# Kernel optimization log

Measured on AMD Instinct MI355X. Metric: run time of the kernel, lower is better.

Reference implementation:

```python
import jax, jax.numpy as jnp
import numpy as np

N_AE = 512
N_DE = 256
N = 100000
NUM_SEG = 1024
EPS = 1e-5


def setup_inputs() -> dict:
    key = jax.random.key(0)
    ks = jax.random.split(key, 20)
    d_in1 = 2 * N_AE + N_DE  # 1280
    inp = {
        "x": jax.random.normal(ks[0], (N, 2 * N_AE), dtype=jnp.float32),
        "dist_feat": jax.random.normal(ks[1], (N, N_DE), dtype=jnp.float32),
        "atom_idx": jax.random.randint(ks[2], (N,), 0, 100, dtype=jnp.int32),
        "ele_idx": jax.random.randint(ks[3], (N,), 0, NUM_SEG, dtype=jnp.int32),
        # layer 1 params
        "l1_w": jax.random.normal(ks[4], (d_in1, N_AE), dtype=jnp.float32) * (1.0 / np.sqrt(d_in1)),
        "l1_b": jnp.zeros((N_AE,), dtype=jnp.float32),
        "l1_g": jnp.ones((N_AE,), dtype=jnp.float32),
        "l1_be": jnp.zeros((N_AE,), dtype=jnp.float32),
        # layer 2 params (same input width: 2*n_ae + n_de)
        "l2_w": jax.random.normal(ks[5], (d_in1, N_AE), dtype=jnp.float32) * (1.0 / np.sqrt(d_in1)),
        "l2_b": jnp.zeros((N_AE,), dtype=jnp.float32),
        "l2_g": jnp.ones((N_AE,), dtype=jnp.float32),
        "l2_be": jnp.zeros((N_AE,), dtype=jnp.float32),
        # final fc + bn
        "f_w": jax.random.normal(ks[6], (2 * N_AE, N_AE), dtype=jnp.float32) * (1.0 / np.sqrt(2 * N_AE)),
        "f_b": jnp.zeros((N_AE,), dtype=jnp.float32),
        "f_g": jnp.ones((N_AE,), dtype=jnp.float32),
        "f_be": jnp.zeros((N_AE,), dtype=jnp.float32),
    }
    return inp


def _bn(h, gamma, beta):
    # BatchNorm1d in training mode: batch stats, biased variance
    m = jnp.mean(h, axis=0)
    v = jnp.mean(jnp.square(h - m), axis=0)
    return gamma * (h - m) * jax.lax.rsqrt(v + EPS) + beta


def _dist_layer(x_cat, ele_idx, w, b, gamma, beta):
    h = jax.nn.relu(_bn(x_cat @ w + b, gamma, beta))  # [N, n_ae]
    sums = jax.ops.segment_sum(h, ele_idx, num_segments=NUM_SEG)  # [S, n_ae]
    cnt = jax.ops.segment_sum(jnp.ones((h.shape[0],), h.dtype), ele_idx, num_segments=NUM_SEG)
    mean = sums / jnp.maximum(cnt, 1.0)[:, None]
    return jnp.concatenate([h, mean[ele_idx]], axis=1)  # [N, 2*n_ae]


def reference(x, dist_feat, atom_idx, ele_idx,
              l1_w, l1_b, l1_g, l1_be,
              l2_w, l2_b, l2_g, l2_be,
              f_w, f_b, f_g, f_be):
    h = _dist_layer(jnp.concatenate([x, dist_feat], axis=1), ele_idx, l1_w, l1_b, l1_g, l1_be)
    h = _dist_layer(jnp.concatenate([h, dist_feat], axis=1), ele_idx, l2_w, l2_b, l2_g, l2_be)
    out = jax.nn.relu(_bn(h @ f_w + f_b, f_g, f_be))  # [N, n_ae]
    return out
```

## Files before the change

### kernel.cpp

```cpp
#include <hip/hip_runtime.h>
#include <stdint.h>
#include <stdio.h>

#define NOUT 512
#define NSEG 1024

typedef unsigned short u16;
typedef __attribute__((ext_vector_type(4))) float f32x4;
typedef __attribute__((ext_vector_type(8))) short s16x8;
typedef __attribute__((ext_vector_type(4))) unsigned short u16x4;

__device__ __forceinline__ u16 f2b(float f) {
  union { float f; uint32_t u; } v; v.f = f;
  uint32_t r = v.u + 0x7FFFu + ((v.u >> 16) & 1u);
  return (u16)(r >> 16);
}
__device__ __forceinline__ float b2f(u16 b) {
  union { uint32_t u; float f; } v; v.u = ((uint32_t)b) << 16;
  return v.f;
}

typedef __attribute__((address_space(1))) const void GAS;
typedef __attribute__((address_space(3))) void LAS;
__device__ __forceinline__ void llds16(const void* g, void* l) {
  __builtin_amdgcn_global_load_lds((GAS*)g, (LAS*)l, 16, 0, 0);
}

__global__ void k_cast2(const float* __restrict__ x, u16* __restrict__ xb, long n4x,
                        const float* __restrict__ d, u16* __restrict__ db, long n4d) {
  long i0 = blockIdx.x * (long)blockDim.x + threadIdx.x;
  long stride = (long)gridDim.x * blockDim.x;
  for (long i = i0; i < n4x; i += stride) {
    float4 v = reinterpret_cast<const float4*>(x)[i];
    u16x4 o;
    o.x = f2b(v.x); o.y = f2b(v.y); o.z = f2b(v.z); o.w = f2b(v.w);
    reinterpret_cast<u16x4*>(xb)[i] = o;
  }
  for (long i = i0; i < n4d; i += stride) {
    float4 v = reinterpret_cast<const float4*>(d)[i];
    u16x4 o;
    o.x = f2b(v.x); o.y = f2b(v.y); o.z = f2b(v.z); o.w = f2b(v.w);
    reinterpret_cast<u16x4*>(db)[i] = o;
  }
}

__global__ void k_wtcastT3(const float* __restrict__ w0, u16* __restrict__ o0,
                           const float* __restrict__ w1, u16* __restrict__ o1,
                           const float* __restrict__ w2, u16* __restrict__ o2) {
  __shared__ float tile[32][33];
  int z = blockIdx.z;
  const float* w = z == 0 ? w0 : (z == 1 ? w1 : w2);
  u16* out = z == 0 ? o0 : (z == 1 ? o1 : o2);
  int K = z == 2 ? 1024 : 1280;
  int k0 = blockIdx.x * 32, c0 = blockIdx.y * 32;
  if (k0 >= K) return;
  int t = threadIdx.x;
  int rr = t >> 5, cc = t & 31;
#pragma unroll
  for (int p = 0; p < 4; ++p)
    tile[p * 8 + rr][cc] = w[(long)(k0 + p * 8 + rr) * NOUT + c0 + cc];
  __syncthreads();
#pragma unroll
  for (int p = 0; p < 4; ++p)
    out[(long)(c0 + p * 8 + rr) * K + k0 + cc] = f2b(tile[cc][p * 8 + rr]);
}

__global__ void k_hist(const int* __restrict__ ele, int* __restrict__ cnt, int N) {
  int i = blockIdx.x * blockDim.x + threadIdx.x;
  int stride = gridDim.x * blockDim.x;
  for (; i < N; i += stride) atomicAdd(&cnt[ele[i]], 1);
}

__global__ void k_scan(const int* __restrict__ cnt, int* __restrict__ off) {
  __shared__ int tmp[NSEG];
  int t = threadIdx.x;
  tmp[t] = cnt[t];
  __syncthreads();
  for (int o = 1; o < NSEG; o <<= 1) {
    int add = (t >= o) ? tmp[t - o] : 0;
    __syncthreads();
    tmp[t] += add;
    __syncthreads();
  }
  off[t] = tmp[t] - cnt[t];
}

__global__ void k_scatter(const int* __restrict__ ele, const int* __restrict__ off,
                          int* __restrict__ fill, int* __restrict__ rows, int N) {
  int i = blockIdx.x * blockDim.x + threadIdx.x;
  int stride = gridDim.x * blockDim.x;
  for (; i < N; i += stride) {
    int e = ele[i];
    int p = atomicAdd(&fill[e], 1);
    rows[off[e] + p] = i;
  }
}

__global__ void k_bnseg(const u16* __restrict__ hp, u16* __restrict__ h, u16* __restrict__ mean,
                        const float* __restrict__ stats, const float* __restrict__ g,
                        const float* __restrict__ be, float invM,
                        const int* __restrict__ off, const int* __restrict__ cnt,
                        const int* __restrict__ rows) {
  int s = blockIdx.x;
  int c0 = 2 * threadIdx.x;
  int n = cnt[s], o = off[s];
  float m0 = stats[c0] * invM, m1 = stats[c0 + 1] * invM;
  float v0 = stats[NOUT + c0] * invM - m0 * m0;
  float v1 = stats[NOUT + c0 + 1] * invM - m1 * m1;
  float a0 = g[c0] * rsqrtf(v0 + 1e-5f);
  float a1 = g[c0 + 1] * rsqrtf(v1 + 1e-5f);
  float cc0 = be[c0] - a0 * m0;
  float cc1 = be[c0 + 1] - a1 * m1;
  float s0 = 0.f, s1 = 0.f;
#pragma unroll 2
  for (int j = 0; j < n; ++j) {
    int r = rows[o + j];
    uint32_t v = *reinterpret_cast<const uint32_t*>(&hp[(long)r * NOUT + c0]);
    float h0 = fmaxf(a0 * b2f((u16)(v & 0xffff)) + cc0, 0.f);
    float h1 = fmaxf(a1 * b2f((u16)(v >> 16)) + cc1, 0.f);
    s0 += h0; s1 += h1;
    *reinterpret_cast<uint32_t*>(&h[(long)r * NOUT + c0]) =
        ((uint32_t)f2b(h1) << 16) | (uint32_t)f2b(h0);
  }
  float inv = 1.f / fmaxf((float)n, 1.f);
  *reinterpret_cast<uint32_t*>(&mean[(long)s * NOUT + c0]) =
      ((uint32_t)f2b(s1 * inv) << 16) | (uint32_t)f2b(s0 * inv);
}

__global__ void k_final(const u16* __restrict__ hp, float* __restrict__ out,
                        const float* __restrict__ stats, const float* __restrict__ g,
                        const float* __restrict__ be, float invM, long n4) {
  __shared__ float sA[NOUT], sC[NOUT];
  for (int c = threadIdx.x; c < NOUT; c += blockDim.x) {
    float m = stats[c] * invM;
    float v = stats[NOUT + c] * invM - m * m;
    float a = g[c] * rsqrtf(v + 1e-5f);
    sA[c] = a;
    sC[c] = be[c] - a * m;
  }
  __syncthreads();
  long i = blockIdx.x * (long)blockDim.x + threadIdx.x;
  long stride = (long)gridDim.x * blockDim.x;
  for (; i < n4; i += stride) {
    u16x4 v = reinterpret_cast<const u16x4*>(hp)[i];
    int c0 = (int)((i * 4) & (NOUT - 1));
    float4 a = *reinterpret_cast<const float4*>(&sA[c0]);
    float4 c = *reinterpret_cast<const float4*>(&sC[c0]);
    float4 o;
    o.x = fmaxf(a.x * b2f(v.x) + c.x, 0.f);
    o.y = fmaxf(a.y * b2f(v.y) + c.y, 0.f);
    o.z = fmaxf(a.z * b2f(v.z) + c.z, 0.f);
    o.w = fmaxf(a.w * b2f(v.w) + c.w, 0.f);
    reinterpret_cast<float4*>(out)[i] = o;
  }
}

__global__ __launch_bounds__(256, 4) void k_gemm(
    const u16* p0, const u16* p1, int e0, int w0, int w1, int g0, int g1,
    const int* __restrict__ ele,
    const u16* __restrict__ wbt, int ldb, int e0b, int bskip,
    const float* __restrict__ tab, int addtab,
    u16* __restrict__ outp, float* __restrict__ outf, int wf32,
    float* __restrict__ csum, float* __restrict__ csq, int dostats,
    int M, int K) {
  __shared__ __align__(16) u16 As[2 * 4096];
  __shared__ __align__(16) u16 Bs[2 * 4096];

  int nwg = gridDim.x;
  int orig = blockIdx.x;
  int q = nwg >> 3, r8 = nwg & 7;
  int xcd = orig & 7, loc = orig >> 3;
  int bid = (xcd < r8 ? xcd * (q + 1) : r8 * (q + 1) + (xcd - r8) * q) + loc;
  int mt = bid >> 2, ct = bid & 3;
  int brow = mt * 128, bcol = ct * 128;

  int tid = (int)threadIdx.x;
  int lane = tid & 63;
  int wid = tid >> 6;
  int wr = wid >> 1, wc = wid & 1;
  int l15 = lane & 15, kg = lane >> 4;

  int srow = tid >> 2;
  int soct = ((tid & 3) ^ ((srow >> 1) & 3)) * 8;

  int gr0 = brow + srow, gr1 = gr0 + 64;
  int gr0c = gr0 < M ? gr0 : M - 1;
  int gr1c = gr1 < M ? gr1 : M - 1;
  int el0 = ele[gr0c], el1 = ele[gr1c];

  const u16* a00 = p0 + (long)(g0 ? el0 : gr0c) * w0 + soct;
  const u16* a01 = p1 + (long)(g1 ? el0 : gr0c) * w1 + soct - e0;
  const u16* a10 = p0 + (long)(g0 ? el1 : gr1c) * w0 + soct;
  const u16* a11 = p1 + (long)(g1 ? el1 : gr1c) * w1 + soct - e0;

  const u16* b0p = wbt + (long)(bcol + srow) * ldb + soct;
  const u16* b1p = wbt + (long)(bcol + srow + 64) * ldb + soct;

  int xoct = (kg ^ ((l15 >> 1) & 3)) * 8;
  int aro = (wr * 64 + l15) * 32 + xoct;
  int bro = (wc * 64 + l15) * 32 + xoct;

  f32x4 acc[4][4];
#pragma unroll
  for (int m = 0; m < 4; ++m)
#pragma unroll
    for (int n = 0; n < 4; ++n)
#pragma unroll
      for (int j = 0; j < 4; ++j) acc[m][n][j] = 0.f;

  int KT = K >> 5;
  int dst = wid * 512;

  auto stage = [&](int tt, int buf) {
    int k0 = tt << 5;
    const u16* sa0 = k0 < e0 ? a00 : a01;
    const u16* sa1 = k0 < e0 ? a10 : a11;
    int bo = k0 + (k0 >= e0b ? bskip : 0);
    int ab = buf * 4096 + dst;
    llds16(sa0 + k0, &As[ab]);
    llds16(sa1 + k0, &As[ab + 2048]);
    llds16(b0p + bo, &Bs[ab]);
    llds16(b1p + bo, &Bs[ab + 2048]);
  };

  stage(0, 0);
  __syncthreads();

  for (int t = 0; t < KT; ++t) {
    int cur = t & 1;
    if (t + 1 < KT) stage(t + 1, cur ^ 1);
    __builtin_amdgcn_sched_barrier(0);
    const u16* Ab = &As[cur * 4096];
    const u16* Bb = &Bs[cur * 4096];
    s16x8 af[4], bf[4];
#pragma unroll
    for (int m = 0; m < 4; ++m)
      af[m] = *reinterpret_cast<const s16x8*>(&Ab[m * 512 + aro]);
#pragma unroll
    for (int n = 0; n < 4; ++n)
      bf[n] = *reinterpret_cast<const s16x8*>(&Bb[n * 512 + bro]);
#pragma unroll
    for (int m = 0; m < 4; ++m)
#pragma unroll
      for (int n = 0; n < 4; ++n)
        acc[m][n] = __builtin_amdgcn_mfma_f32_16x16x32_bf16(af[m], bf[n], acc[m][n], 0, 0, 0);
    __syncthreads();
  }

  float sums[4] = {0.f, 0.f, 0.f, 0.f}, sqs[4] = {0.f, 0.f, 0.f, 0.f};
#pragma unroll
  for (int m = 0; m < 4; ++m) {
    int row0 = brow + wr * 64 + m * 16 + kg * 4;
#pragma unroll
    for (int j = 0; j < 4; ++j) {
      int r = row0 + j;
      if (r < M) {
        long rb = (long)r * NOUT;
        long tb = addtab ? (long)ele[r] * NOUT : 0;
#pragma unroll
        for (int n = 0; n < 4; ++n) {
          int col = bcol + wc * 64 + n * 16 + l15;
          float v = acc[m][n][j];
          if (addtab) v += tab[tb + col];
          if (wf32) outf[rb + col] = v;
          else outp[rb + col] = f2b(v);
          sums[n] += v;
          sqs[n] += v * v;
        }
      }
    }
  }
  if (dostats) {
#pragma unroll
    for (int n = 0; n < 4; ++n) {
      sums[n] += __shfl_xor(sums[n], 16);
      sums[n] += __shfl_xor(sums[n], 32);
      sqs[n] += __shfl_xor(sqs[n], 16);
      sqs[n] += __shfl_xor(sqs[n], 32);
    }
    if (kg == 0) {
#pragma unroll
      for (int n = 0; n < 4; ++n) {
        int col = bcol + wc * 64 + n * 16 + l15;
        atomicAdd(&csum[col], sums[n]);
        atomicAdd(&csq[col], sqs[n]);
      }
    }
  }
}

extern "C" void kernel_launch(void* const* d_in, const int* in_sizes, int n_in,
                              void* d_out, int out_size, void* d_ws, size_t ws_size,
                              hipStream_t stream) {
  const float* x    = (const float*)d_in[0];
  const float* dist = (const float*)d_in[1];
  const int* ele    = (const int*)d_in[3];
  const float* l1w  = (const float*)d_in[4];
  const float* l1g  = (const float*)d_in[6];
  const float* l1be = (const float*)d_in[7];
  const float* l2w  = (const float*)d_in[8];
  const float* l2g  = (const float*)d_in[10];
  const float* l2be = (const float*)d_in[11];
  const float* fw   = (const float*)d_in[12];
  const float* fg   = (const float*)d_in[14];
  const float* fbe  = (const float*)d_in[15];

  int N = in_sizes[0] / 1024;
  float* out = (float*)d_out;
  u16* xbf = (u16*)d_out;

  int MT = (N + 127) / 128;

  char* w = (char*)d_ws;
  auto alloc = [&](size_t bytes) {
    char* p = w;
    w += (bytes + 255) & ~(size_t)255;
    return p;
  };
  u16* dist_bf = (u16*)alloc((size_t)N * 256 * 2);
  u16* hp      = (u16*)alloc((size_t)N * NOUT * 2);
  u16* h       = (u16*)alloc((size_t)N * NOUT * 2);
  u16* mean    = (u16*)alloc((size_t)NSEG * NOUT * 2);
  u16* w1bt    = (u16*)alloc((size_t)NOUT * 1280 * 2);
  u16* w2bt    = (u16*)alloc((size_t)NOUT * 1280 * 2);
  u16* fbt     = (u16*)alloc((size_t)NOUT * 1024 * 2);
  float* mc2   = (float*)alloc((size_t)NSEG * NOUT * 4);
  float* mc3   = (float*)alloc((size_t)NSEG * NOUT * 4);
  char* zz0    = w;
  int* seg_cnt = (int*)alloc(NSEG * 4);
  int* seg_fill = (int*)alloc(NSEG * 4);
  float* stats1 = (float*)alloc(NOUT * 2 * 4);
  float* stats2 = (float*)alloc(NOUT * 2 * 4);
  float* stats3 = (float*)alloc(NOUT * 2 * 4);
  size_t zzlen = (size_t)(w - zz0);
  int* seg_off = (int*)alloc(NSEG * 4);
  int* rows    = (int*)alloc((size_t)N * 4);

  size_t need = (size_t)(w - (char*)d_ws);
  if (need > ws_size) {
    fprintf(stderr, "kernel_launch: ws too small: need %zu have %zu\n", need, ws_size);
    return;
  }

  long n4x = (long)N * 1024 / 4;
  long n4d = (long)N * 256 / 4;
  long n4h = (long)N * NOUT / 4;
  int gemmGrid = MT * 4;
  int mcGrid = (NSEG / 128) * 4;
  float invM = 1.0f / (float)N;

  k_cast2<<<4096, 256, 0, stream>>>(x, xbf, n4x, dist, dist_bf, n4d);
  dim3 wtg(1280 / 32, NOUT / 32, 3);
  k_wtcastT3<<<wtg, 256, 0, stream>>>(l1w, w1bt, l2w, w2bt, fw, fbt);
  hipMemsetAsync(zz0, 0, zzlen, stream);

  k_hist<<<512, 256, 0, stream>>>(ele, seg_cnt, N);
  k_scan<<<1, NSEG, 0, stream>>>(seg_cnt, seg_off);
  k_scatter<<<512, 256, 0, stream>>>(ele, seg_off, seg_fill, rows, N);

  k_gemm<<<gemmGrid, 256, 0, stream>>>(xbf, dist_bf, 1024, 1024, 256, 0, 0, ele,
                                       w1bt, 1280, 1280, 0, mc2, 0,
                                       hp, mc2, 0, stats1, stats1 + NOUT, 1, N, 1280);
  k_bnseg<<<NSEG, 256, 0, stream>>>(hp, h, mean, stats1, l1g, l1be, invM,
                                    seg_off, seg_cnt, rows);

  k_gemm<<<mcGrid, 256, 0, stream>>>(mean, mean, 512, 512, 512, 0, 0, ele,
                                     w2bt + 512, 1280, 512, 0, mc2, 0,
                                     hp, mc2, 1, stats2, stats2 + NOUT, 0, NSEG, 512);
  k_gemm<<<gemmGrid, 256, 0, stream>>>(h, dist_bf, 512, 512, 256, 0, 0, ele,
                                       w2bt, 1280, 512, 512, mc2, 1,
                                       hp, mc2, 0, stats2, stats2 + NOUT, 1, N, 768);
  k_bnseg<<<NSEG, 256, 0, stream>>>(hp, h, mean, stats2, l2g, l2be, invM,
                                    seg_off, seg_cnt, rows);

  k_gemm<<<mcGrid, 256, 0, stream>>>(mean, mean, 512, 512, 512, 0, 0, ele,
                                     fbt + 512, 1024, 512, 0, mc3, 0,
                                     hp, mc3, 1, stats3, stats3 + NOUT, 0, NSEG, 512);
  k_gemm<<<gemmGrid, 256, 0, stream>>>(h, h, 512, 512, 512, 0, 0, ele,
                                       fbt, 1024, 512, 0, mc3, 1,
                                       hp, mc3, 0, stats3, stats3 + NOUT, 1, N, 512);
  k_final<<<4096, 256, 0, stream>>>(hp, out, stats3, fg, fbe, invM, n4h);
}
```

Before: 932.1 us.

## Fuse fp32-to-bf16 cast of layer-1 inputs into the first GEMM's A-tile load

Drops the separate pass that converts x to bf16. The first GEMM now loads fp32 rows of x and dist_feat straight into LDS with a swizzled layout and converts them to bf16 while building MFMA fragments. This removes a full write and re-read of the 100000x1024 bf16 copy of x. In exchange the A tile takes twice the LDS, occupancy drops to 3 waves per SIMD, and every block does extra conversion ALU work (repeated across the 4 column tiles).

```diff
diff --git a/kernel.cpp b/kernel.cpp
--- a/kernel.cpp
+++ b/kernel.cpp
@@ -26,17 +26,10 @@
   __builtin_amdgcn_global_load_lds((GAS*)g, (LAS*)l, 16, 0, 0);
 }
 
-__global__ void k_cast2(const float* __restrict__ x, u16* __restrict__ xb, long n4x,
-                        const float* __restrict__ d, u16* __restrict__ db, long n4d) {
-  long i0 = blockIdx.x * (long)blockDim.x + threadIdx.x;
+__global__ void k_castd(const float* __restrict__ d, u16* __restrict__ db, long n4d) {
+  long i = blockIdx.x * (long)blockDim.x + threadIdx.x;
   long stride = (long)gridDim.x * blockDim.x;
-  for (long i = i0; i < n4x; i += stride) {
-    float4 v = reinterpret_cast<const float4*>(x)[i];
-    u16x4 o;
-    o.x = f2b(v.x); o.y = f2b(v.y); o.z = f2b(v.z); o.w = f2b(v.w);
-    reinterpret_cast<u16x4*>(xb)[i] = o;
-  }
-  for (long i = i0; i < n4d; i += stride) {
+  for (; i < n4d; i += stride) {
     float4 v = reinterpret_cast<const float4*>(d)[i];
     u16x4 o;
     o.x = f2b(v.x); o.y = f2b(v.y); o.z = f2b(v.z); o.w = f2b(v.w);
@@ -155,16 +148,19 @@
   }
 }
 
-__global__ __launch_bounds__(256, 4) void k_gemm(
-    const u16* p0, const u16* p1, int e0, int w0, int w1, int g0, int g1,
+template <int FA>
+__global__ __launch_bounds__(256, FA ? 3 : 4) void k_gemm(
+    const u16* p0, const u16* p1, const float* fx, const float* fd,
+    int e0, int w0, int w1, int g0, int g1,
     const int* __restrict__ ele,
     const u16* __restrict__ wbt, int ldb, int e0b, int bskip,
     const float* __restrict__ tab, int addtab,
     u16* __restrict__ outp, float* __restrict__ outf, int wf32,
     float* __restrict__ csum, float* __restrict__ csq, int dostats,
     int M, int K) {
-  __shared__ __align__(16) u16 As[2 * 4096];
+  __shared__ __align__(16) u16 AsU[FA ? 2 * 8192 : 2 * 4096];
   __shared__ __align__(16) u16 Bs[2 * 4096];
+  float* AsF = reinterpret_cast<float*>(AsU);
 
   int nwg = gridDim.x;
   int orig = blockIdx.x;
@@ -183,15 +179,28 @@
   int srow = tid >> 2;
   int soct = ((tid & 3) ^ ((srow >> 1) & 3)) * 8;
 
-  int gr0 = brow + srow, gr1 = gr0 + 64;
-  int gr0c = gr0 < M ? gr0 : M - 1;
-  int gr1c = gr1 < M ? gr1 : M - 1;
-  int el0 = ele[gr0c], el1 = ele[gr1c];
-
-  const u16* a00 = p0 + (long)(g0 ? el0 : gr0c) * w0 + soct;
-  const u16* a01 = p1 + (long)(g1 ? el0 : gr0c) * w1 + soct - e0;
-  const u16* a10 = p0 + (long)(g0 ? el1 : gr1c) * w0 + soct;
-  const u16* a11 = p1 + (long)(g1 ? el1 : gr1c) * w1 + soct - e0;
+  const u16 *a00 = nullptr, *a01 = nullptr, *a10 = nullptr, *a11 = nullptr;
+  const float *fxa[4], *fda[4];
+  if constexpr (FA) {
+    int swz4 = ((lane & 7) ^ ((lane >> 3) & 7)) * 4;
+#pragma unroll
+    for (int i = 0; i < 4; ++i) {
+      int c = wid * 4 + i;
+      int gr = brow + c * 8 + (lane >> 3);
+      if (gr >= M) gr = M - 1;
+      fxa[i] = fx + (long)gr * w0 + swz4;
+      fda[i] = fd + (long)gr * w1 + swz4;
+    }
+  } else {
+    int gr0 = brow + srow, gr1 = gr0 + 64;
+    int gr0c = gr0 < M ? gr0 : M - 1;
+    int gr1c = gr1 < M ? gr1 : M - 1;
+    int el0 = (g0 | g1) ? ele[gr0c] : 0, el1 = (g0 | g1) ? ele[gr1c] : 0;
+    a00 = p0 + (long)(g0 ? el0 : gr0c) * w0 + soct;
+    a01 = p1 + (long)(g1 ? el0 : gr0c) * w1 + soct - e0;
+    a10 = p0 + (long)(g0 ? el1 : gr1c) * w0 + soct;
+    a11 = p1 + (long)(g1 ? el1 : gr1c) * w1 + soct - e0;
+  }
 
   const u16* b0p = wbt + (long)(bcol + srow) * ldb + soct;
   const u16* b1p = wbt + (long)(bcol + srow + 64) * ldb + soct;
@@ -213,14 +222,27 @@
 
   auto stage = [&](int tt, int buf) {
     int k0 = tt << 5;
-    const u16* sa0 = k0 < e0 ? a00 : a01;
-    const u16* sa1 = k0 < e0 ? a10 : a11;
+    if constexpr (FA) {
+      if (k0 < e0) {
+#pragma unroll
+        for (int i = 0; i < 4; ++i)
+          llds16(fxa[i] + k0, &AsF[buf * 4096 + (wid * 4 + i) * 256]);
+      } else {
+#pragma unroll
+        for (int i = 0; i < 4; ++i)
+          llds16(fda[i] + (k0 - e0), &AsF[buf * 4096 + (wid * 4 + i) * 256]);
+      }
+    } else {
+      const u16* sa0 = k0 < e0 ? a00 : a01;
+      const u16* sa1 = k0 < e0 ? a10 : a11;
+      int ab = buf * 4096 + dst;
+      llds16(sa0 + k0, &AsU[ab]);
+      llds16(sa1 + k0, &AsU[ab + 2048]);
+    }
     int bo = k0 + (k0 >= e0b ? bskip : 0);
-    int ab = buf * 4096 + dst;
-    llds16(sa0 + k0, &As[ab]);
-    llds16(sa1 + k0, &As[ab + 2048]);
-    llds16(b0p + bo, &Bs[ab]);
-    llds16(b1p + bo, &Bs[ab + 2048]);
+    int bb = buf * 4096 + dst;
+    llds16(b0p + bo, &Bs[bb]);
+    llds16(b1p + bo, &Bs[bb + 2048]);
   };
 
   stage(0, 0);
@@ -230,12 +252,29 @@
     int cur = t & 1;
     if (t + 1 < KT) stage(t + 1, cur ^ 1);
     __builtin_amdgcn_sched_barrier(0);
-    const u16* Ab = &As[cur * 4096];
     const u16* Bb = &Bs[cur * 4096];
     s16x8 af[4], bf[4];
-#pragma unroll
-    for (int m = 0; m < 4; ++m)
-      af[m] = *reinterpret_cast<const s16x8*>(&Ab[m * 512 + aro]);
+    if constexpr (FA) {
+      int rbase = cur * 4096;
+      int u1 = (2 * kg) ^ (l15 & 7);
+#pragma unroll
+      for (int m = 0; m < 4; ++m) {
+        int ro = rbase + (wr * 64 + m * 16 + l15) * 32;
+        f32x4 lo = *reinterpret_cast<const f32x4*>(&AsF[ro + u1 * 4]);
+        f32x4 hi = *reinterpret_cast<const f32x4*>(&AsF[ro + (u1 ^ 1) * 4]);
+        s16x8 a;
+        a[0] = (short)f2b(lo[0]); a[1] = (short)f2b(lo[1]);
+        a[2] = (short)f2b(lo[2]); a[3] = (short)f2b(lo[3]);
+        a[4] = (short)f2b(hi[0]); a[5] = (short)f2b(hi[1]);
+        a[6] = (short)f2b(hi[2]); a[7] = (short)f2b(hi[3]);
+        af[m] = a;
+      }
+    } else {
+      const u16* Ab = &AsU[cur * 4096];
+#pragma unroll
+      for (int m = 0; m < 4; ++m)
+        af[m] = *reinterpret_cast<const s16x8*>(&Ab[m * 512 + aro]);
+    }
 #pragma unroll
     for (int n = 0; n < 4; ++n)
       bf[n] = *reinterpret_cast<const s16x8*>(&Bb[n * 512 + bro]);
@@ -307,7 +346,6 @@
 
   int N = in_sizes[0] / 1024;
   float* out = (float*)d_out;
-  u16* xbf = (u16*)d_out;
 
   int MT = (N + 127) / 128;
 
@@ -342,14 +380,13 @@
     return;
   }
 
-  long n4x = (long)N * 1024 / 4;
   long n4d = (long)N * 256 / 4;
   long n4h = (long)N * NOUT / 4;
   int gemmGrid = MT * 4;
   int mcGrid = (NSEG / 128) * 4;
   float invM = 1.0f / (float)N;
 
-  k_cast2<<<4096, 256, 0, stream>>>(x, xbf, n4x, dist, dist_bf, n4d);
+  k_castd<<<2048, 256, 0, stream>>>(dist, dist_bf, n4d);
   dim3 wtg(1280 / 32, NOUT / 32, 3);
   k_wtcastT3<<<wtg, 256, 0, stream>>>(l1w, w1bt, l2w, w2bt, fw, fbt);
   hipMemsetAsync(zz0, 0, zzlen, stream);
@@ -358,26 +395,31 @@
   k_scan<<<1, NSEG, 0, stream>>>(seg_cnt, seg_off);
   k_scatter<<<512, 256, 0, stream>>>(ele, seg_off, seg_fill, rows, N);
 
-  k_gemm<<<gemmGrid, 256, 0, stream>>>(xbf, dist_bf, 1024, 1024, 256, 0, 0, ele,
-                                       w1bt, 1280, 1280, 0, mc2, 0,
-                                       hp, mc2, 0, stats1, stats1 + NOUT, 1, N, 1280);
+  k_gemm<1><<<gemmGrid, 256, 0, stream>>>(nullptr, nullptr, x, dist,
+                                          1024, 1024, 256, 0, 0, ele,
+                                          w1bt, 1280, 1280, 0, mc2, 0,
+                                          hp, mc2, 0, stats1, stats1 + NOUT, 1, N, 1280);
   k_bnseg<<<NSEG, 256, 0, stream>>>(hp, h, mean, stats1, l1g, l1be, invM,
                                     seg_off, seg_cnt, rows);
 
-  k_gemm<<<mcGrid, 256, 0, stream>>>(mean, mean, 512, 512, 512, 0, 0, ele,
-                                     w2bt + 512, 1280, 512, 0, mc2, 0,
-                                     hp, mc2, 1, stats2, stats2 + NOUT, 0, NSEG, 512);
-  k_gemm<<<gemmGrid, 256, 0, stream>>>(h, dist_bf, 512, 512, 256, 0, 0, ele,
-                                       w2bt, 1280, 512, 512, mc2, 1,
-                                       hp, mc2, 0, stats2, stats2 + NOUT, 1, N, 768);
+  k_gemm<0><<<mcGrid, 256, 0, stream>>>(mean, mean, nullptr, nullptr,
+                                        512, 512, 512, 0, 0, ele,
+                                        w2bt + 512, 1280, 512, 0, mc2, 0,
+                                        hp, mc2, 1, stats2, stats2 + NOUT, 0, NSEG, 512);
+  k_gemm<0><<<gemmGrid, 256, 0, stream>>>(h, dist_bf, nullptr, nullptr,
+                                          512, 512, 256, 0, 0, ele,
+                                          w2bt, 1280, 512, 512, mc2, 1,
+                                          hp, mc2, 0, stats2, stats2 + NOUT, 1, N, 768);
   k_bnseg<<<NSEG, 256, 0, stream>>>(hp, h, mean, stats2, l2g, l2be, invM,
                                     seg_off, seg_cnt, rows);
 
-  k_gemm<<<mcGrid, 256, 0, stream>>>(mean, mean, 512, 512, 512, 0, 0, ele,
-                                     fbt + 512, 1024, 512, 0, mc3, 0,
-                                     hp, mc3, 1, stats3, stats3 + NOUT, 0, NSEG, 512);
-  k_gemm<<<gemmGrid, 256, 0, stream>>>(h, h, 512, 512, 512, 0, 0, ele,
-                                       fbt, 1024, 512, 0, mc3, 1,
-                                       hp, mc3, 0, stats3, stats3 + NOUT, 1, N, 512);
+  k_gemm<0><<<mcGrid, 256, 0, stream>>>(mean, mean, nullptr, nullptr,
+                                        512, 512, 512, 0, 0, ele,
+                                        fbt + 512, 1024, 512, 0, mc3, 0,
+                                        hp, mc3, 1, stats3, stats3 + NOUT, 0, NSEG, 512);
+  k_gemm<0><<<gemmGrid, 256, 0, stream>>>(h, h, nullptr, nullptr,
+                                          512, 512, 512, 0, 0, ele,
+                                          fbt, 1024, 512, 0, mc3, 1,
+                                          hp, mc3, 0, stats3, stats3 + NOUT, 1, N, 512);
   k_final<<<4096, 256, 0, stream>>>(hp, out, stats3, fg, fbe, invM, n4h);
 }
```

Result: no change. 932.0 us (-0.0%).
